# Performance work log

Hardware: AMD Instinct MI355X
Metric: run time of the kernel (lower is better)

Reference implementation:

```python
import jax, jax.numpy as jnp
import numpy as np

DIM, HEADS = 1024, 16
HD = DIM // HEADS  # head_dim = 64
EPS = 1e-5


def setup_inputs() -> dict:
    key = jax.random.key(0)
    ks = jax.random.split(key, 8)
    B, N = 2, 2048
    x = jax.random.normal(ks[0], (B, N, DIM), dtype=jnp.float32)
    # RoPE table: [N, HD//2, 2] = (cos, sin) per position/freq
    inv_freq = 1.0 / (10000.0 ** (jnp.arange(0, HD, 2, dtype=jnp.float32) / HD))  # [HD//2]
    angles = jnp.arange(N, dtype=jnp.float32)[:, None] * inv_freq[None, :]        # [N, HD//2]
    freq_cis = jnp.stack([jnp.cos(angles), jnp.sin(angles)], axis=-1)             # [N, HD//2, 2]
    s = 0.02
    Wqkv = jax.random.normal(ks[1], (DIM, 3 * DIM), dtype=jnp.float32) * s
    ln_q_g = jnp.ones((HD,), jnp.float32)
    ln_q_b = jnp.zeros((HD,), jnp.float32)
    ln_k_g = jnp.ones((HD,), jnp.float32)
    ln_k_b = jnp.zeros((HD,), jnp.float32)
    Wproj = jax.random.normal(ks[2], (DIM, DIM), dtype=jnp.float32) * s
    bproj = jnp.zeros((DIM,), jnp.float32)
    return {"x": x, "freq_cis": freq_cis, "Wqkv": Wqkv,
            "ln_q_g": ln_q_g, "ln_q_b": ln_q_b, "ln_k_g": ln_k_g, "ln_k_b": ln_k_b,
            "Wproj": Wproj, "bproj": bproj}


def _layernorm(t, g, b):
    mu = jnp.mean(t, axis=-1, keepdims=True)
    var = jnp.mean(jnp.square(t - mu), axis=-1, keepdims=True)
    return (t - mu) * jax.lax.rsqrt(var + EPS) * g + b


def _rope(t, cos, sin):
    # t: [b, n, h, hd]; pairs are interleaved (even=real, odd=imag)
    b, n, h, hd = t.shape
    tr = jnp.transpose(t[..., 0::2], (0, 2, 1, 3))  # [b, h, n, hd//2]
    ti = jnp.transpose(t[..., 1::2], (0, 2, 1, 3))
    out_r = tr * cos - ti * sin
    out_i = tr * sin + ti * cos
    return jnp.stack([out_r, out_i], axis=-1).reshape(b, h, n, hd)  # [b, h, n, hd]


def reference(x, freq_cis, Wqkv, ln_q_g, ln_q_b, ln_k_g, ln_k_b, Wproj, bproj):
    B, N, _ = x.shape
    qkv = (x @ Wqkv).reshape(B, N, 3, HEADS, HD)  # split is outermost in the packed dim
    q, k, v = qkv[:, :, 0], qkv[:, :, 1], qkv[:, :, 2]  # [b, n, h, hd]
    q = _layernorm(q, ln_q_g, ln_q_b)
    k = _layernorm(k, ln_k_g, ln_k_b)
    cos = freq_cis[None, None, :, :, 0]  # [1, 1, n, hd//2]
    sin = freq_cis[None, None, :, :, 1]
    q = _rope(q, cos, sin)  # [b, h, n, hd]
    k = _rope(k, cos, sin)
    v = jnp.transpose(v, (0, 2, 1, 3))  # [b, h, n, hd]
    scores = jnp.einsum('bhqd,bhkd->bhqk', q, k) * (1.0 / np.sqrt(HD))
    attn = jax.nn.softmax(scores, axis=-1)
    out = jnp.einsum('bhqk,bhkd->bhqd', attn, v)
    out = jnp.transpose(out, (0, 2, 1, 3)).reshape(B, N, HEADS * HD)
    return out @ Wproj + bproj
```

## Files before the change

### kernel.cpp

```cpp
#include <hip/hip_runtime.h>

typedef __bf16 bf16_t;
typedef bf16_t bf16x8 __attribute__((ext_vector_type(8)));
typedef bf16_t bf16x4 __attribute__((ext_vector_type(4)));
typedef float f32x4 __attribute__((ext_vector_type(4)));
typedef short s16x4 __attribute__((ext_vector_type(4)));

typedef __attribute__((address_space(1))) void* as1_void;
typedef __attribute__((address_space(3))) void* as3_void;

static constexpr int kDim   = 1024;
static constexpr int kHeads = 16;
static constexpr int kHd    = 64;
static constexpr int kBatch = 2;
static constexpr int kSeq   = 2048;
static constexpr int kM     = kBatch * kSeq;
static constexpr int kNqkv  = 3 * kDim;
static constexpr float kQScale = 0.125f * 1.4426950408889634f;
static constexpr float kFixedMax = 16.0f;

__device__ __forceinline__ void gld_lds16(const bf16_t* g, bf16_t* l) {
  __builtin_amdgcn_global_load_lds((as1_void)(void*)const_cast<bf16_t*>(g),
                                   (as3_void)(void*)l, 16, 0, 0);
}

__device__ __forceinline__ float fexp2(float x) {
#if __has_builtin(__builtin_amdgcn_exp2f)
  return __builtin_amdgcn_exp2f(x);
#else
  float r;
  asm("v_exp_f32 %0, %1" : "=v"(r) : "v"(x));
  return r;
#endif
}

__device__ __forceinline__ unsigned cvtpk_bf16(float lo, float hi) {
  unsigned r;
  asm("v_cvt_pk_bf16_f32 %0, %1, %2" : "=v"(r) : "v"(lo), "v"(hi));
  return r;
}

__global__ __launch_bounds__(256) void prep(const float* __restrict__ x, bf16_t* __restrict__ xb,
                                            const float* __restrict__ Wqkv, bf16_t* __restrict__ WqkvT,
                                            const float* __restrict__ Wproj, bf16_t* __restrict__ WprojT) {
  __shared__ float tile[32][33];
  const int bid = blockIdx.x, tid = threadIdx.x;
  if (bid < 1024) {
#pragma unroll
    for (int j = 0; j < 4; ++j) {
      const int i = bid * 1024 + j * 256 + tid;
      const float4 f = ((const float4*)x)[i];
      bf16x4 o;
      o[0] = (bf16_t)f.x; o[1] = (bf16_t)f.y; o[2] = (bf16_t)f.z; o[3] = (bf16_t)f.w;
      ((bf16x4*)xb)[i] = o;
    }
    return;
  }
  const float* in; bf16_t* out; int R, C, t;
  if (bid < 4096) { in = Wqkv;  out = WqkvT;  R = kDim; C = kNqkv; t = bid - 1024; }
  else            { in = Wproj; out = WprojT; R = kDim; C = kDim;  t = bid - 4096; }
  const int ntx = C / 32;
  const int c0 = (t % ntx) * 32, r0 = (t / ntx) * 32;
  const int tx = tid & 31, ty = tid >> 5;
#pragma unroll
  for (int j = 0; j < 4; ++j)
    tile[ty + 8 * j][tx] = in[(size_t)(r0 + ty + 8 * j) * C + (c0 + tx)];
  __syncthreads();
#pragma unroll
  for (int j = 0; j < 4; ++j)
    out[(size_t)(c0 + ty + 8 * j) * R + (r0 + tx)] = (bf16_t)tile[tx][ty + 8 * j];
}

__global__ __launch_bounds__(256) void gemm_proj_fused(const bf16_t* __restrict__ p0,
                                                       const bf16_t* __restrict__ p1,
                                                       const float* __restrict__ rs,
                                                       const bf16_t* __restrict__ Bt,
                                                       float* __restrict__ Cout,
                                                       const float* __restrict__ bias) {
  const int N = kDim, K = kDim;
  __shared__ __align__(16) bf16_t lA[2][2048];
  __shared__ __align__(16) bf16_t lB[2][4096];
  __shared__ float invt[1024];
  const int tid  = threadIdx.x;
  const int w    = tid >> 6, lane = tid & 63;
  const int quad = lane >> 4, l16 = lane & 15;
  const int m0 = blockIdx.y * 64, n0 = blockIdx.x * 128;

#pragma unroll
  for (int j = 0; j < 4; ++j) {
    const int e = tid * 4 + j;
    const int i = e >> 4, h = e & 15;
    const int row = m0 + i;
    const int b = row >> 11, r = row & 2047;
    const int bh = b * kHeads + h;
    invt[e] = 1.f / (rs[(size_t)bh * kSeq + r] + rs[(size_t)(32 + bh) * kSeq + r]);
  }

  const int strow = tid >> 2;
  const int stcol = (tid & 3) * 8;
  const int swcol = (((tid & 3) ^ ((strow >> 1) & 3))) * 8;
  const size_t aoff = (size_t)(m0 + strow) * K + stcol;
  const bf16_t* gB = Bt + (size_t)(n0 + strow) * K + swcol;
  const int rdx = ((l16 >> 1) & 3);

  f32x4 acc[4][2];
#pragma unroll
  for (int i = 0; i < 4; ++i)
#pragma unroll
    for (int j = 0; j < 2; ++j)
#pragma unroll
      for (int r = 0; r < 4; ++r) acc[i][j][r] = 0.f;

  auto stageB = [&](int buf, int k0) {
    gld_lds16(gB + k0, &lB[buf][w * 512]);
    gld_lds16(gB + (size_t)64 * K + k0, &lB[buf][2048 + w * 512]);
  };
  auto writeA = [&](int buf, int kb, bf16x8 a0, bf16x8 a1) {
    const float inv = invt[strow * 16 + (kb >> 1)];
    unsigned u[4];
#pragma unroll
    for (int p = 0; p < 4; ++p)
      u[p] = cvtpk_bf16(((float)a0[2 * p] + (float)a1[2 * p]) * inv,
                        ((float)a0[2 * p + 1] + (float)a1[2 * p + 1]) * inv);
    uint4 uu = {u[0], u[1], u[2], u[3]};
    *(uint4*)(&lA[buf][strow * 32 + swcol]) = uu;
  };

  const int nK = K >> 5;
  bf16x8 a0 = *(const bf16x8*)(p0 + aoff);
  bf16x8 a1 = *(const bf16x8*)(p1 + aoff);
  stageB(0, 0);
  __syncthreads();
  writeA(0, 0, a0, a1);
  __syncthreads();

  for (int kb = 0; kb < nK; ++kb) {
    const int cur = kb & 1;
    if (kb + 1 < nK) {
      a0 = *(const bf16x8*)(p0 + aoff + (kb + 1) * 32);
      a1 = *(const bf16x8*)(p1 + aoff + (kb + 1) * 32);
      stageB(cur ^ 1, (kb + 1) * 32);
    }
    bf16x8 af[4], bfr[2];
#pragma unroll
    for (int mt = 0; mt < 4; ++mt)
      af[mt] = *(const bf16x8*)(&lA[cur][(mt * 16 + l16) * 32 + (quad ^ rdx) * 8]);
#pragma unroll
    for (int nt = 0; nt < 2; ++nt)
      bfr[nt] = *(const bf16x8*)(&lB[cur][(w * 32 + nt * 16 + l16) * 32 + (quad ^ rdx) * 8]);
#pragma unroll
    for (int mt = 0; mt < 4; ++mt)
#pragma unroll
      for (int nt = 0; nt < 2; ++nt)
        acc[mt][nt] = __builtin_amdgcn_mfma_f32_16x16x32_bf16(af[mt], bfr[nt], acc[mt][nt], 0, 0, 0);
    if (kb + 1 < nK) writeA(cur ^ 1, kb + 1, a0, a1);
    __syncthreads();
  }

#pragma unroll
  for (int mt = 0; mt < 4; ++mt)
#pragma unroll
    for (int nt = 0; nt < 2; ++nt)
#pragma unroll
      for (int r = 0; r < 4; ++r) {
        const int row = m0 + mt * 16 + quad * 4 + r;
        const int col = n0 + w * 32 + nt * 16 + l16;
        Cout[(size_t)row * N + col] = acc[mt][nt][r] + bias[col];
      }
}

__global__ __launch_bounds__(256, 3) void gemm_qkv_fused(
    const bf16_t* __restrict__ A, const bf16_t* __restrict__ Bt,
    const float* __restrict__ freq,
    const float* __restrict__ gq, const float* __restrict__ bq,
    const float* __restrict__ gk, const float* __restrict__ bk,
    bf16_t* __restrict__ Q, bf16_t* __restrict__ Kout, bf16_t* __restrict__ Vt) {
  __shared__ __align__(16) char smem[49152];
  bf16_t* lA = (bf16_t*)smem;
  bf16_t* lB = lA + 12288;
  const int tid  = threadIdx.x;
  const int w    = tid >> 6, lane = tid & 63;
  const int quad = lane >> 4, l16 = lane & 15;
  const int wm = w >> 1, wn = w & 1;
  const int m0 = blockIdx.y * 128, n0 = blockIdx.x * 128;
  const int K = kDim;

  const int strow = tid >> 2;
  const int swcol = (((tid & 3) ^ ((strow >> 1) & 3))) * 8;
  const bf16_t* gA = A  + (size_t)(m0 + strow) * K + swcol;
  const bf16_t* gB = Bt + (size_t)(n0 + strow) * K + swcol;

  f32x4 acc[4][4];
#pragma unroll
  for (int i = 0; i < 4; ++i)
#pragma unroll
    for (int j = 0; j < 4; ++j)
#pragma unroll
      for (int r = 0; r < 4; ++r) acc[i][j][r] = 0.f;

  auto stage = [&](int buf, int k0) {
    gld_lds16(gA + k0,                  lA + buf * 4096 + w * 512);
    gld_lds16(gA + (size_t)64 * K + k0, lA + buf * 4096 + 2048 + w * 512);
    gld_lds16(gB + k0,                  lB + buf * 4096 + w * 512);
    gld_lds16(gB + (size_t)64 * K + k0, lB + buf * 4096 + 2048 + w * 512);
  };

  const int rdx = ((l16 >> 1) & 3);
  const int ia_ = (wm * 64 + l16) * 32 + (quad ^ rdx) * 8;
  const int ib_ = (wn * 64 + l16) * 32 + (quad ^ rdx) * 8;

  auto body = [&](int bufEl) {
    bf16x8 af[4], bfr[4];
#pragma unroll
    for (int mt = 0; mt < 4; ++mt)
      af[mt] = *(const bf16x8*)(lA + bufEl + ia_ + mt * 512);
#pragma unroll
    for (int nt = 0; nt < 4; ++nt)
      bfr[nt] = *(const bf16x8*)(lB + bufEl + ib_ + nt * 512);
#pragma unroll
    for (int mt = 0; mt < 4; ++mt)
#pragma unroll
      for (int nt = 0; nt < 4; ++nt)
        acc[mt][nt] = __builtin_amdgcn_mfma_f32_16x16x32_bf16(af[mt], bfr[nt], acc[mt][nt], 0, 0, 0);
  };

  stage(0, 0);
  stage(1, 32);

  for (int g = 0; g < 10; ++g) {
    asm volatile("s_waitcnt vmcnt(4)" ::: "memory");
    __builtin_amdgcn_sched_barrier(0);
    __builtin_amdgcn_s_barrier();
    stage(2, (3 * g + 2) * 32);
    body(0);

    asm volatile("s_waitcnt vmcnt(4)" ::: "memory");
    __builtin_amdgcn_sched_barrier(0);
    __builtin_amdgcn_s_barrier();
    stage(0, (3 * g + 3) * 32);
    body(4096);

    asm volatile("s_waitcnt vmcnt(4)" ::: "memory");
    __builtin_amdgcn_sched_barrier(0);
    __builtin_amdgcn_s_barrier();
    stage(1, (3 * g + 4) * 32);
    body(8192);
  }
  asm volatile("s_waitcnt vmcnt(4)" ::: "memory");
  __builtin_amdgcn_sched_barrier(0);
  __builtin_amdgcn_s_barrier();
  body(0);
  asm volatile("s_waitcnt vmcnt(0)" ::: "memory");
  __builtin_amdgcn_sched_barrier(0);
  __builtin_amdgcn_s_barrier();
  body(4096);

  const int mat = n0 >> 10;
  const int cin = (n0 & 1023) + wn * 64;
  const int h   = cin >> 6;
  const int bb  = m0 >> 11;
  const int bh  = bb * kHeads + h;
  const int nrow0 = (m0 & 2047) + wm * 64;

  if (mat == 2) {
#pragma unroll
    for (int mt = 0; mt < 4; ++mt)
#pragma unroll
      for (int nt = 0; nt < 4; ++nt) {
        bf16x4 pk;
#pragma unroll
        for (int r = 0; r < 4; ++r) pk[r] = (bf16_t)acc[mt][nt][r];
        const int d = nt * 16 + l16;
        *(bf16x4*)(Vt + ((size_t)bh * kHd + d) * kSeq + nrow0 + mt * 16 + quad * 4) = pk;
      }
    return;
  }

  __syncthreads();
  float* fsm = (float*)smem;
  {
    const int row = tid >> 1, half = tid & 1;
    const float4* src = (const float4*)(freq + ((size_t)(m0 & 2047) + row) * 64 + half * 32);
    float4* dst4 = (float4*)(fsm + row * 68 + half * 32);
#pragma unroll
    for (int j = 0; j < 8; ++j) dst4[j] = src[j];
  }
  __syncthreads();

  const float* gv_ = (mat == 0) ? gq : gk;
  const float* bv_ = (mat == 0) ? bq : bk;
  float gv[4], bv[4];
#pragma unroll
  for (int nt = 0; nt < 4; ++nt) { gv[nt] = gv_[nt * 16 + l16]; bv[nt] = bv_[nt * 16 + l16]; }
  bf16_t* dst = (mat == 0) ? Q : Kout;
  const float sgn = (l16 & 1) ? 1.f : -1.f;
  const float scl = (mat == 0) ? kQScale : 1.f;

#pragma unroll
  for (int mt = 0; mt < 4; ++mt) {
    float mu[4], inv[4];
#pragma unroll
    for (int r = 0; r < 4; ++r) {
      float s = acc[mt][0][r] + acc[mt][1][r] + acc[mt][2][r] + acc[mt][3][r];
      s += __shfl_xor(s, 1); s += __shfl_xor(s, 2);
      s += __shfl_xor(s, 4); s += __shfl_xor(s, 8);
      mu[r] = s * (1.f / 64.f);
    }
#pragma unroll
    for (int r = 0; r < 4; ++r) {
      float vs = 0.f;
#pragma unroll
      for (int nt = 0; nt < 4; ++nt) {
        const float dd = acc[mt][nt][r] - mu[r];
        vs += dd * dd;
      }
      vs += __shfl_xor(vs, 1); vs += __shfl_xor(vs, 2);
      vs += __shfl_xor(vs, 4); vs += __shfl_xor(vs, 8);
      inv[r] = rsqrtf(vs * (1.f / 64.f) + 1e-5f);
    }
#pragma unroll
    for (int nt = 0; nt < 4; ++nt) {
#pragma unroll
      for (int r = 0; r < 4; ++r) {
        const float y = (acc[mt][nt][r] - mu[r]) * inv[r] * gv[nt] + bv[nt];
        const float part = __shfl_xor(y, 1);
        const int mloc = wm * 64 + mt * 16 + quad * 4 + r;
        const float2 cs = *(const float2*)(fsm + mloc * 68 + ((nt * 16 + l16) & ~1));
        const float outv = (y * cs.x + sgn * part * cs.y) * scl;
        dst[((size_t)bh * kSeq + nrow0 + mt * 16 + quad * 4 + r) * kHd + nt * 16 + l16] =
            (bf16_t)outv;
      }
    }
  }
}

__global__ __launch_bounds__(256, 4) void flash_attn16(const bf16_t* __restrict__ Q,
                                                       const bf16_t* __restrict__ K,
                                                       const bf16_t* __restrict__ Vt,
                                                       bf16_t* __restrict__ Op0,
                                                       bf16_t* __restrict__ Op1,
                                                       float* __restrict__ rsum) {
  __shared__ __align__(16) bf16_t lK[2][4096];
  __shared__ __align__(16) bf16_t lV[2][4096];
  const int tid  = threadIdx.x;
  const int w    = tid >> 6, lane = tid & 63;
  const int quad = lane >> 4, l16 = lane & 15;
  const int bh = blockIdx.x & 31;
  const int t2 = blockIdx.x >> 5;
  const int qb = t2 & 15;
  const int sp = t2 >> 4;
  const int b = bh >> 4, h = bh & 15;
  const int q0 = qb * 128 + w * 32;
  const int kv0 = sp * (kSeq / 2);
  const bf16_t* Qb = Q  + (size_t)bh * kSeq * kHd;
  const bf16_t* Kb = K  + (size_t)bh * kSeq * kHd + (size_t)kv0 * kHd;
  const bf16_t* Vb = Vt + (size_t)bh * kHd * kSeq + kv0;

  bf16x8 qf[2][2];
#pragma unroll
  for (int nt = 0; nt < 2; ++nt)
#pragma unroll
    for (int ks = 0; ks < 2; ++ks)
      qf[nt][ks] = *(const bf16x8*)(Qb + (size_t)(q0 + nt * 16 + l16) * kHd + ks * 32 + quad * 8);

  bf16x8 ones8;
#pragma unroll
  for (int j = 0; j < 8; ++j) ones8[j] = (bf16_t)((l16 == 0) ? 1.0f : 0.0f);

  const int r0s = (w * 2 + 0) * 8 + (lane >> 3);
  const int r1s = (w * 2 + 1) * 8 + (lane >> 3);
  const int ch  = lane & 7;
  const bf16_t* kS0 = Kb + (size_t)r0s * kHd + (ch ^ (r0s & 7)) * 8;
  const bf16_t* kS1 = Kb + (size_t)r1s * kHd + (ch ^ (r1s & 7)) * 8;
  const bf16_t* vS0 = Vb + (size_t)r0s * kSeq + (ch ^ (r0s & 7)) * 8;
  const bf16_t* vS1 = Vb + (size_t)r1s * kSeq + (ch ^ (r1s & 7)) * 8;
  bf16_t* dK0 = &lK[0][(w * 2 + 0) * 512];
  bf16_t* dK1 = &lK[0][(w * 2 + 1) * 512];
  bf16_t* dV0 = &lV[0][(w * 2 + 0) * 512];
  bf16_t* dV1 = &lV[0][(w * 2 + 1) * 512];

  auto stage = [&](int buf, int tile) {
    gld_lds16(kS0 + (size_t)tile * 4096, dK0 + buf * 4096);
    gld_lds16(kS1 + (size_t)tile * 4096, dK1 + buf * 4096);
    gld_lds16(vS0 + (size_t)tile * 64,   dV0 + buf * 4096);
    gld_lds16(vS1 + (size_t)tile * 64,   dV1 + buf * 4096);
  };

  int kix[2][2][2], vix[2][4];
#pragma unroll
  for (int pr = 0; pr < 2; ++pr) {
#pragma unroll
    for (int sub = 0; sub < 2; ++sub) {
      const int krow = pr * 32 + (l16 >> 2) * 8 + sub * 4 + (l16 & 3);
      const int swl  = sub * 4 + (l16 & 3);
      kix[pr][sub][0] = krow * 64 + (quad ^ swl) * 8;
      kix[pr][sub][1] = krow * 64 + ((4 + quad) ^ swl) * 8;
    }
#pragma unroll
    for (int ntd = 0; ntd < 4; ++ntd) {
      const int vrow = ntd * 16 + l16;
      vix[pr][ntd] = vrow * 64 + ((pr * 4 + quad) ^ (vrow & 7)) * 8;
    }
  }
  const bf16_t* lKf = &lK[0][0];
  const bf16_t* lVf = &lV[0][0];

  f32x4 o[4][2];
  f32x4 osum[2];
#pragma unroll
  for (int nt = 0; nt < 2; ++nt) {
#pragma unroll
    for (int r = 0; r < 4; ++r) osum[nt][r] = 0.f;
#pragma unroll
    for (int ntd = 0; ntd < 4; ++ntd)
#pragma unroll
      for (int r = 0; r < 4; ++r) o[ntd][nt][r] = 0.f;
  }

  auto body = [&](int bufEl) {
#pragma unroll
    for (int pr = 0; pr < 2; ++pr) {
      unsigned pbu[2][2][2];
#pragma unroll
      for (int sub = 0; sub < 2; ++sub) {
        const bf16x8 kf0 = *(const bf16x8*)(lKf + bufEl + kix[pr][sub][0]);
        const bf16x8 kf1 = *(const bf16x8*)(lKf + bufEl + kix[pr][sub][1]);
        __builtin_amdgcn_s_setprio(1);
#pragma unroll
        for (int nt = 0; nt < 2; ++nt) {
          f32x4 st;
#pragma unroll
          for (int r = 0; r < 4; ++r) st[r] = -kFixedMax;
          st = __builtin_amdgcn_mfma_f32_16x16x32_bf16(kf0, qf[nt][0], st, 0, 0, 0);
          st = __builtin_amdgcn_mfma_f32_16x16x32_bf16(kf1, qf[nt][1], st, 0, 0, 0);
          pbu[sub][nt][0] = cvtpk_bf16(fexp2(st[0]), fexp2(st[1]));
          pbu[sub][nt][1] = cvtpk_bf16(fexp2(st[2]), fexp2(st[3]));
        }
        __builtin_amdgcn_s_setprio(0);
      }
      bf16x8 va[4];
#pragma unroll
      for (int ntd = 0; ntd < 4; ++ntd)
        va[ntd] = *(const bf16x8*)(lVf + bufEl + vix[pr][ntd]);
      __builtin_amdgcn_s_setprio(1);
#pragma unroll
      for (int nt = 0; nt < 2; ++nt) {
        uint4 u = {pbu[0][nt][0], pbu[0][nt][1], pbu[1][nt][0], pbu[1][nt][1]};
        const bf16x8 pfr = __builtin_bit_cast(bf16x8, u);
#pragma unroll
        for (int ntd = 0; ntd < 4; ++ntd)
          o[ntd][nt] = __builtin_amdgcn_mfma_f32_16x16x32_bf16(va[ntd], pfr, o[ntd][nt], 0, 0, 0);
        osum[nt] = __builtin_amdgcn_mfma_f32_16x16x32_bf16(ones8, pfr, osum[nt], 0, 0, 0);
      }
      __builtin_amdgcn_s_setprio(0);
    }
  };

  stage(0, 0);
  __syncthreads();

  for (int t = 0; t < 8; ++t) {
    stage(1, 2 * t + 1);
    body(0);
    __syncthreads();
    if (t < 7) stage(0, 2 * t + 2);
    body(4096);
    __syncthreads();
  }

  if (quad == 0) {
#pragma unroll
    for (int nt = 0; nt < 2; ++nt)
      rsum[((size_t)sp * 32 + bh) * kSeq + q0 + nt * 16 + l16] = osum[nt][0];
  }

  bf16_t* op = sp ? Op1 : Op0;
#pragma unroll
  for (int nt = 0; nt < 2; ++nt) {
    const int row = q0 + nt * 16 + l16;
#pragma unroll
    for (int ntd = 0; ntd < 4; ++ntd) {
      bf16x4 ov;
#pragma unroll
      for (int r = 0; r < 4; ++r) ov[r] = (bf16_t)o[ntd][nt][r];
      *(bf16x4*)(op + ((size_t)(b * kSeq + row)) * kDim + h * kHd + ntd * 16 + quad * 4) = ov;
    }
  }
}

extern "C" void kernel_launch(void* const* d_in, const int* in_sizes, int n_in,
                              void* d_out, int out_size, void* d_ws, size_t ws_size,
                              hipStream_t stream) {
  const float* x     = (const float*)d_in[0];
  const float* freq  = (const float*)d_in[1];
  const float* Wqkv  = (const float*)d_in[2];
  const float* gq    = (const float*)d_in[3];
  const float* bq    = (const float*)d_in[4];
  const float* gk    = (const float*)d_in[5];
  const float* bk    = (const float*)d_in[6];
  const float* Wproj = (const float*)d_in[7];
  const float* bproj = (const float*)d_in[8];
  float* out = (float*)d_out;

  char* ws = (char*)d_ws;
  bf16_t* xb     = (bf16_t*)(ws + 0);
  bf16_t* WqkvT  = (bf16_t*)(ws + 8388608);
  bf16_t* WprojT = (bf16_t*)(ws + 14680064);
  bf16_t* Qb     = (bf16_t*)(ws + 16777216);
  bf16_t* Kb     = (bf16_t*)(ws + 25165824);
  bf16_t* Vtb    = (bf16_t*)(ws + 33554432);
  bf16_t* part0  = (bf16_t*)(ws + 41943040);
  bf16_t* part1  = (bf16_t*)(ws + 0);
  float*  rsum   = (float*)(ws + 8388608);

  prep<<<dim3(5120), dim3(256), 0, stream>>>(x, xb, Wqkv, WqkvT, Wproj, WprojT);
  gemm_qkv_fused<<<dim3(kNqkv / 128, kM / 128), dim3(256), 0, stream>>>(
      xb, WqkvT, freq, gq, bq, gk, bk, Qb, Kb, Vtb);
  flash_attn16<<<dim3((kSeq / 128) * 2 * kBatch * kHeads), dim3(256), 0, stream>>>(
      Qb, Kb, Vtb, part0, part1, rsum);
  gemm_proj_fused<<<dim3(kDim / 128, kM / 64), dim3(256), 0, stream>>>(
      part0, part1, rsum, WprojT, out, bproj);
}
```

Before: 196.6 us.

## Triple-buffer K/V tiles in flash attention with vmcnt-based waits

```diff
diff --git a/kernel.cpp b/kernel.cpp
--- a/kernel.cpp
+++ b/kernel.cpp
@@ -334,14 +334,14 @@
   }
 }
 
-__global__ __launch_bounds__(256, 4) void flash_attn16(const bf16_t* __restrict__ Q,
+__global__ __launch_bounds__(256, 3) void flash_attn20(const bf16_t* __restrict__ Q,
                                                        const bf16_t* __restrict__ K,
                                                        const bf16_t* __restrict__ Vt,
                                                        bf16_t* __restrict__ Op0,
                                                        bf16_t* __restrict__ Op1,
                                                        float* __restrict__ rsum) {
-  __shared__ __align__(16) bf16_t lK[2][4096];
-  __shared__ __align__(16) bf16_t lV[2][4096];
+  __shared__ __align__(16) bf16_t lK[3][4096];
+  __shared__ __align__(16) bf16_t lV[3][4096];
   const int tid  = threadIdx.x;
   const int w    = tid >> 6, lane = tid & 63;
   const int quad = lane >> 4, l16 = lane & 15;
@@ -457,16 +457,48 @@
   };
 
   stage(0, 0);
-  __syncthreads();
-
-  for (int t = 0; t < 8; ++t) {
-    stage(1, 2 * t + 1);
+  stage(1, 1);
+
+  for (int g = 0; g < 4; ++g) {
+    asm volatile("s_waitcnt vmcnt(4)" ::: "memory");
+    __builtin_amdgcn_sched_barrier(0);
+    __builtin_amdgcn_s_barrier();
+    stage(2, 3 * g + 2);
     body(0);
-    __syncthreads();
-    if (t < 7) stage(0, 2 * t + 2);
+
+    asm volatile("s_waitcnt vmcnt(4)" ::: "memory");
+    __builtin_amdgcn_sched_barrier(0);
+    __builtin_amdgcn_s_barrier();
+    stage(0, 3 * g + 3);
     body(4096);
-    __syncthreads();
-  }
+
+    asm volatile("s_waitcnt vmcnt(4)" ::: "memory");
+    __builtin_amdgcn_sched_barrier(0);
+    __builtin_amdgcn_s_barrier();
+    stage(1, 3 * g + 4);
+    body(8192);
+  }
+  asm volatile("s_waitcnt vmcnt(4)" ::: "memory");
+  __builtin_amdgcn_sched_barrier(0);
+  __builtin_amdgcn_s_barrier();
+  stage(2, 14);
+  body(0);
+
+  asm volatile("s_waitcnt vmcnt(4)" ::: "memory");
+  __builtin_amdgcn_sched_barrier(0);
+  __builtin_amdgcn_s_barrier();
+  stage(0, 15);
+  body(4096);
+
+  asm volatile("s_waitcnt vmcnt(4)" ::: "memory");
+  __builtin_amdgcn_sched_barrier(0);
+  __builtin_amdgcn_s_barrier();
+  body(8192);
+
+  asm volatile("s_waitcnt vmcnt(0)" ::: "memory");
+  __builtin_amdgcn_sched_barrier(0);
+  __builtin_amdgcn_s_barrier();
+  body(0);
 
   if (quad == 0) {
 #pragma unroll
@@ -516,7 +548,7 @@
   prep<<<dim3(5120), dim3(256), 0, stream>>>(x, xb, Wqkv, WqkvT, Wproj, WprojT);
   gemm_qkv_fused<<<dim3(kNqkv / 128, kM / 128), dim3(256), 0, stream>>>(
       xb, WqkvT, freq, gq, bq, gk, bk, Qb, Kb, Vtb);
-  flash_attn16<<<dim3((kSeq / 128) * 2 * kBatch * kHeads), dim3(256), 0, stream>>>(
+  flash_attn20<<<dim3((kSeq / 128) * 2 * kBatch * kHeads), dim3(256), 0, stream>>>(
       Qb, Kb, Vtb, part0, part1, rsum);
   gemm_proj_fused<<<dim3(kDim / 128, kM / 64), dim3(256), 0, stream>>>(
       part0, part1, rsum, WprojT, out, bproj);
```

Measured after the change: 198.7 us. About the same (+1.0%).

## Triple-buffer projection GEMM with explicit waitcnt and barrier scheduling

Applied to the files above, without the earlier changes.

```diff
diff --git a/kernel.cpp b/kernel.cpp
--- a/kernel.cpp
+++ b/kernel.cpp
@@ -78,8 +78,8 @@
                                                        float* __restrict__ Cout,
                                                        const float* __restrict__ bias) {
   const int N = kDim, K = kDim;
-  __shared__ __align__(16) bf16_t lA[2][2048];
-  __shared__ __align__(16) bf16_t lB[2][4096];
+  __shared__ __align__(16) bf16_t lA[3][2048];
+  __shared__ __align__(16) bf16_t lB[3][4096];
   __shared__ float invt[1024];
   const int tid  = threadIdx.x;
   const int w    = tid >> 6, lane = tid & 63;
@@ -111,11 +111,14 @@
 #pragma unroll
       for (int r = 0; r < 4; ++r) acc[i][j][r] = 0.f;
 
-  auto stageB = [&](int buf, int k0) {
-    gld_lds16(gB + k0, &lB[buf][w * 512]);
-    gld_lds16(gB + (size_t)64 * K + k0, &lB[buf][2048 + w * 512]);
-  };
-  auto writeA = [&](int buf, int kb, bf16x8 a0, bf16x8 a1) {
+  bf16_t* lA0 = &lA[0][0];
+  bf16_t* lB0 = &lB[0][0];
+
+  auto stageB = [&](int bbufEl, int k0) {
+    gld_lds16(gB + k0, lB0 + bbufEl + w * 512);
+    gld_lds16(gB + (size_t)64 * K + k0, lB0 + bbufEl + 2048 + w * 512);
+  };
+  auto writeA = [&](int abufEl, int kb, bf16x8 a0, bf16x8 a1) {
     const float inv = invt[strow * 16 + (kb >> 1)];
     unsigned u[4];
 #pragma unroll
@@ -123,39 +126,72 @@
       u[p] = cvtpk_bf16(((float)a0[2 * p] + (float)a1[2 * p]) * inv,
                         ((float)a0[2 * p + 1] + (float)a1[2 * p + 1]) * inv);
     uint4 uu = {u[0], u[1], u[2], u[3]};
-    *(uint4*)(&lA[buf][strow * 32 + swcol]) = uu;
-  };
-
-  const int nK = K >> 5;
+    *(uint4*)(lA0 + abufEl + strow * 32 + swcol) = uu;
+  };
+  auto body = [&](int abufEl, int bbufEl) {
+    bf16x8 af[4], bfr[2];
+#pragma unroll
+    for (int mt = 0; mt < 4; ++mt)
+      af[mt] = *(const bf16x8*)(lA0 + abufEl + (mt * 16 + l16) * 32 + (quad ^ rdx) * 8);
+#pragma unroll
+    for (int nt = 0; nt < 2; ++nt)
+      bfr[nt] = *(const bf16x8*)(lB0 + bbufEl + (w * 32 + nt * 16 + l16) * 32 + (quad ^ rdx) * 8);
+#pragma unroll
+    for (int mt = 0; mt < 4; ++mt)
+#pragma unroll
+      for (int nt = 0; nt < 2; ++nt)
+        acc[mt][nt] = __builtin_amdgcn_mfma_f32_16x16x32_bf16(af[mt], bfr[nt], acc[mt][nt], 0, 0, 0);
+  };
+
   bf16x8 a0 = *(const bf16x8*)(p0 + aoff);
   bf16x8 a1 = *(const bf16x8*)(p1 + aoff);
   stageB(0, 0);
   __syncthreads();
   writeA(0, 0, a0, a1);
-  __syncthreads();
-
-  for (int kb = 0; kb < nK; ++kb) {
-    const int cur = kb & 1;
-    if (kb + 1 < nK) {
-      a0 = *(const bf16x8*)(p0 + aoff + (kb + 1) * 32);
-      a1 = *(const bf16x8*)(p1 + aoff + (kb + 1) * 32);
-      stageB(cur ^ 1, (kb + 1) * 32);
-    }
-    bf16x8 af[4], bfr[2];
-#pragma unroll
-    for (int mt = 0; mt < 4; ++mt)
-      af[mt] = *(const bf16x8*)(&lA[cur][(mt * 16 + l16) * 32 + (quad ^ rdx) * 8]);
-#pragma unroll
-    for (int nt = 0; nt < 2; ++nt)
-      bfr[nt] = *(const bf16x8*)(&lB[cur][(w * 32 + nt * 16 + l16) * 32 + (quad ^ rdx) * 8]);
-#pragma unroll
-    for (int mt = 0; mt < 4; ++mt)
-#pragma unroll
-      for (int nt = 0; nt < 2; ++nt)
-        acc[mt][nt] = __builtin_amdgcn_mfma_f32_16x16x32_bf16(af[mt], bfr[nt], acc[mt][nt], 0, 0, 0);
-    if (kb + 1 < nK) writeA(cur ^ 1, kb + 1, a0, a1);
-    __syncthreads();
-  }
+  a0 = *(const bf16x8*)(p0 + aoff + 32);
+  a1 = *(const bf16x8*)(p1 + aoff + 32);
+  stageB(4096, 32);
+  asm volatile("s_waitcnt lgkmcnt(0)" ::: "memory");
+  __builtin_amdgcn_sched_barrier(0);
+  __builtin_amdgcn_s_barrier();
+
+  for (int g = 0; g < 10; ++g) {
+    stageB(8192, (3 * g + 2) * 32);
+    body(0, 0);
+    writeA(2048, 3 * g + 1, a0, a1);
+    a0 = *(const bf16x8*)(p0 + aoff + (3 * g + 2) * 32);
+    a1 = *(const bf16x8*)(p1 + aoff + (3 * g + 2) * 32);
+    asm volatile("s_waitcnt lgkmcnt(0)" ::: "memory");
+    asm volatile("s_waitcnt vmcnt(4)" ::: "memory");
+    __builtin_amdgcn_sched_barrier(0);
+    __builtin_amdgcn_s_barrier();
+
+    stageB(0, (3 * g + 3) * 32);
+    body(2048, 4096);
+    writeA(4096, 3 * g + 2, a0, a1);
+    a0 = *(const bf16x8*)(p0 + aoff + (3 * g + 3) * 32);
+    a1 = *(const bf16x8*)(p1 + aoff + (3 * g + 3) * 32);
+    asm volatile("s_waitcnt lgkmcnt(0)" ::: "memory");
+    asm volatile("s_waitcnt vmcnt(4)" ::: "memory");
+    __builtin_amdgcn_sched_barrier(0);
+    __builtin_amdgcn_s_barrier();
+
+    stageB(4096, (3 * g + 4) * 32);
+    body(4096, 8192);
+    writeA(0, 3 * g + 3, a0, a1);
+    a0 = *(const bf16x8*)(p0 + aoff + (3 * g + 4) * 32);
+    a1 = *(const bf16x8*)(p1 + aoff + (3 * g + 4) * 32);
+    asm volatile("s_waitcnt lgkmcnt(0)" ::: "memory");
+    asm volatile("s_waitcnt vmcnt(4)" ::: "memory");
+    __builtin_amdgcn_sched_barrier(0);
+    __builtin_amdgcn_s_barrier();
+  }
+  body(0, 0);
+  writeA(2048, 31, a0, a1);
+  asm volatile("s_waitcnt lgkmcnt(0)" ::: "memory");
+  __builtin_amdgcn_sched_barrier(0);
+  __builtin_amdgcn_s_barrier();
+  body(2048, 4096);
 
 #pragma unroll
   for (int mt = 0; mt < 4; ++mt)
```

New measurement: 202.1 us. 2.8% more time.
